# Kernel tuning notes

Hardware: AMD Instinct MI355X
Metric: run time of the kernel (lower is better)

Reference implementation:

```python
import jax, jax.numpy as jnp
import numpy as np

N = 8192
H_CHANNELS = 2048
HEADS = 16
D = H_CHANNELS // HEADS  # 128


def setup_inputs() -> dict:
    key = jax.random.key(0)
    k1, k2, k3 = jax.random.split(key, 3)
    x0 = jax.random.normal(k1, (N, H_CHANNELS), dtype=jnp.float32)
    # boolean mask: True entries are masked out (set to -inf)
    mask = jax.random.randint(k2, (N, N), 0, 2).astype(jnp.bool_)
    # torch Linear weight layout: [out_features, in_features] = [3*d, h_channels]
    W_qkv = jax.random.normal(k3, (3 * D, H_CHANNELS), dtype=jnp.float32) * (1.0 / np.sqrt(H_CHANNELS))
    return {"x0": x0, "mask": mask, "W_qkv": W_qkv}


def reference(x0, mask, W_qkv):
    # qkv = x0 @ W^T : [N, 3d]
    qkv = x0 @ W_qkv.T
    q, k, v = jnp.split(qkv, 3, axis=-1)          # each [N, d]
    att_logits = (q @ k.T) / D                    # [N, N]  (note: scale is /d, not /sqrt(d))
    att_logits = jnp.where(mask, -jnp.inf, att_logits)
    att = jax.nn.softmax(att_logits, axis=-1)     # [N, N]
    # dropout p=0.0 (eval mode) -> identity
    return att @ v                                # [N, d]
```

## Files before the change

### kernel.cpp

```cpp
#include <hip/hip_runtime.h>
#include <hip/hip_bf16.h>

typedef __attribute__((ext_vector_type(8))) short short8;
typedef __attribute__((ext_vector_type(4))) float f32x4;
typedef __attribute__((ext_vector_type(16))) float f32x16;
typedef __attribute__((ext_vector_type(2))) unsigned int uint2v;

#define NTOK 8192
#define HCH  2048
#define DDIM 128
#define NSPLIT 8
#define KPS   (NTOK / NSPLIT)
#define NITER (KPS / 64)

__device__ __forceinline__ unsigned short f2bf(float f) {
    __hip_bfloat16 h = __float2bfloat16(f);
    return *reinterpret_cast<unsigned short*>(&h);
}
__device__ __forceinline__ unsigned short f2h(float f) {
    _Float16 h = (_Float16)f;
    return *reinterpret_cast<unsigned short*>(&h);
}

__device__ __forceinline__ void gload_lds16(const void* g, void* l) {
    __builtin_amdgcn_global_load_lds(
        reinterpret_cast<const __attribute__((address_space(1))) unsigned int*>(
            reinterpret_cast<uintptr_t>(g)),
        reinterpret_cast<__attribute__((address_space(3))) unsigned int*>(
            reinterpret_cast<uintptr_t>(l)),
        16, 0, 0);
}

__global__ void detect_kernel(const unsigned int* __restrict__ X,
                              const unsigned int* __restrict__ M,
                              int* __restrict__ flags)
{
    const int lane = threadIdx.x & 63;
    unsigned int e = (X[lane] >> 7) & 0xFF;
    unsigned long long hb = __ballot(e >= 110 && e <= 140);

    bool w_ok = true, h_ok = true, b_ok = true;
#pragma unroll
    for (int i = 0; i < 16; i++) {
        unsigned int u = M[lane + 64 * i];
        if (!(u == 0u || u == 1u || u == 0x3F800000u)) w_ok = false;
        unsigned int h0 = u & 0xFFFFu, h1 = u >> 16;
        bool o0 = (h0 == 0u || h0 == 0x3F80u || h0 == 0x3C00u || h0 == 1u);
        bool o1 = (h1 == 0u || h1 == 0x3F80u || h1 == 0x3C00u || h1 == 1u);
        if (!(o0 && o1)) h_ok = false;
        unsigned int b0 = u & 0xFF, b1 = (u >> 8) & 0xFF,
                     b2 = (u >> 16) & 0xFF, b3 = u >> 24;
        if (b0 > 1u || b1 > 1u || b2 > 1u || b3 > 1u) b_ok = false;
    }
    bool allw = __all(w_ok), allh = __all(h_ok), allb = __all(b_ok);
    if (lane == 0) {
        flags[0] = (__popcll(hb) < 32) ? 1 : 0;
        flags[1] = allw ? 0 : (allb ? 1 : (allh ? 2 : 3));
    }
}

__global__ __launch_bounds__(256) void conv_w(
    const void* __restrict__ Wv, const int* __restrict__ flags,
    unsigned short* __restrict__ Wbf)
{
    int t = blockIdx.x * 256 + threadIdx.x;
    size_t off = (size_t)t * 8;
    if (flags[0] != 0) {
        const float* Wf = (const float*)Wv;
        float4 a = *reinterpret_cast<const float4*>(Wf + off);
        float4 b = *reinterpret_cast<const float4*>(Wf + off + 4);
        unsigned short o[8] = { f2bf(a.x), f2bf(a.y), f2bf(a.z), f2bf(a.w),
                                f2bf(b.x), f2bf(b.y), f2bf(b.z), f2bf(b.w) };
        *reinterpret_cast<uint4*>(Wbf + off) = *reinterpret_cast<uint4*>(o);
    } else {
        *reinterpret_cast<uint4*>(Wbf + off) =
            *reinterpret_cast<const uint4*>((const unsigned short*)Wv + off);
    }
}

__global__ __launch_bounds__(256) void conv_x(
    const void* __restrict__ Xv, const int* __restrict__ flags,
    unsigned short* __restrict__ Xbf)
{
    int t = blockIdx.x * 256 + threadIdx.x;
    size_t off = (size_t)t * 8;
    if (flags[0] != 0) {
        const float* Xf = (const float*)Xv;
        float4 a = *reinterpret_cast<const float4*>(Xf + off);
        float4 b = *reinterpret_cast<const float4*>(Xf + off + 4);
        unsigned short o[8] = { f2bf(a.x), f2bf(a.y), f2bf(a.z), f2bf(a.w),
                                f2bf(b.x), f2bf(b.y), f2bf(b.z), f2bf(b.w) };
        *reinterpret_cast<uint4*>(Xbf + off) = *reinterpret_cast<uint4*>(o);
    } else {
        *reinterpret_cast<uint4*>(Xbf + off) =
            *reinterpret_cast<const uint4*>((const unsigned short*)Xv + off);
    }
}

__global__ __launch_bounds__(256) void mask_pack(
    const void* __restrict__ maskv, const int* __restrict__ flags,
    unsigned char* __restrict__ Mp)
{
    const int mmode = flags[1];
    const int NB = NTOK * (NTOK / 8);
    int t0 = blockIdx.x * 256 + threadIdx.x;
    for (int b = t0; b < NB; b += 2048 * 256) {
        unsigned int byte = 0;
        if (mmode == 0) {
            const uint4* p = reinterpret_cast<const uint4*>(
                (const unsigned int*)maskv + (size_t)b * 8);
            uint4 a = p[0], c = p[1];
            byte = (a.x != 0u) | ((a.y != 0u) << 1) | ((a.z != 0u) << 2) | ((a.w != 0u) << 3)
                 | ((c.x != 0u) << 4) | ((c.y != 0u) << 5) | ((c.z != 0u) << 6) | ((c.w != 0u) << 7);
        } else if (mmode == 1) {
            unsigned long long v = *reinterpret_cast<const unsigned long long*>(
                (const unsigned char*)maskv + (size_t)b * 8);
#pragma unroll
            for (int k = 0; k < 8; k++)
                byte |= (((v >> (8 * k)) & 0xFFull) != 0ull) << k;
        } else if (mmode == 2) {
            uint4 a = *reinterpret_cast<const uint4*>(
                (const unsigned short*)maskv + (size_t)b * 8);
            byte = ((a.x & 0xFFFFu) != 0u) | ((a.x >> 16 != 0u) << 1)
                 | (((a.y & 0xFFFFu) != 0u) << 2) | ((a.y >> 16 != 0u) << 3)
                 | (((a.z & 0xFFFFu) != 0u) << 4) | ((a.z >> 16 != 0u) << 5)
                 | (((a.w & 0xFFFFu) != 0u) << 6) | ((a.w >> 16 != 0u) << 7);
        } else {
            byte = ((const unsigned char*)maskv)[b];
        }
        Mp[b] = (unsigned char)byte;
    }
}

__global__ __launch_bounds__(256) void qkv_gemm(
    const unsigned short* __restrict__ Xbf, const unsigned short* __restrict__ Wbf,
    unsigned short* __restrict__ Qb, unsigned short* __restrict__ Kb,
    unsigned short* __restrict__ Vb)
{
    __shared__ unsigned short Wsm[128 * 64];
    __shared__ unsigned short Xsm[32 * 64];
    const int tid  = threadIdx.x;
    const int lane = tid & 63, w = tid >> 6;
    const int c = lane & 15, g = lane >> 4;
    const int q0 = blockIdx.x * 32;
    const int n0 = blockIdx.y * 128;

    f32x4 acc[4];
#pragma unroll
    for (int i = 0; i < 4; i++) acc[i] = (f32x4){0.f, 0.f, 0.f, 0.f};

    const int xrow = tid >> 3, xc8 = tid & 7;
    const int arow = (w & 1) * 16 + c;

    for (int kk = 0; kk < HCH; kk += 64) {
        __syncthreads();
#pragma unroll
        for (int i = 0; i < 4; i++) {
            int cid = tid + 256 * i;
            int n = cid >> 3, c8 = cid & 7;
            gload_lds16(Wbf + (size_t)(n0 + n) * HCH + kk + ((c8 ^ (n & 7)) * 8),
                        &Wsm[cid * 8]);
        }
        gload_lds16(Xbf + (size_t)(q0 + xrow) * HCH + kk + ((xc8 ^ (xrow & 7)) * 8),
                    &Xsm[tid * 8]);
        __syncthreads();
#pragma unroll
        for (int ks = 0; ks < 2; ks++) {
            short8 af = *reinterpret_cast<const short8*>(
                &Xsm[(arow * 8 + ((ks * 4 + g) ^ (c & 7))) * 8]);
#pragma unroll
            for (int nt = 0; nt < 4; nt++) {
                int n = (w >> 1) * 64 + nt * 16 + c;
                short8 bf = *reinterpret_cast<const short8*>(
                    &Wsm[(n * 8 + ((ks * 4 + g) ^ (c & 7))) * 8]);
                acc[nt] = __builtin_amdgcn_mfma_f32_16x16x32_bf16(af, bf, acc[nt], 0, 0, 0);
            }
        }
    }
    unsigned short* dst = (blockIdx.y == 0) ? Qb : (blockIdx.y == 1) ? Kb : Vb;
#pragma unroll
    for (int nt = 0; nt < 4; nt++) {
        int n = (w >> 1) * 64 + nt * 16 + c;
#pragma unroll
        for (int r = 0; r < 4; r++) {
            int rr = q0 + (w & 1) * 16 + g * 4 + r;
            dst[(size_t)rr * DDIM + n] = f2bf(acc[nt][r]);
        }
    }
}

__global__ __launch_bounds__(256) void vtrans(
    const unsigned short* __restrict__ V, unsigned short* __restrict__ VT)
{
    __shared__ unsigned short T[32 * 33];
    const int t = threadIdx.x;
    const int k0 = blockIdx.x * 32, d0 = blockIdx.y * 32;
    {
        int key = t >> 3, dq = (t & 7) * 4;
        ushort4 v = *reinterpret_cast<const ushort4*>(V + (size_t)(k0 + key) * DDIM + d0 + dq);
        T[(dq + 0) * 33 + key] = v.x;
        T[(dq + 1) * 33 + key] = v.y;
        T[(dq + 2) * 33 + key] = v.z;
        T[(dq + 3) * 33 + key] = v.w;
    }
    __syncthreads();
    {
        int d = t >> 3, kq = (t & 7) * 4;
        ushort4 o;
        o.x = T[d * 33 + kq + 0]; o.y = T[d * 33 + kq + 1];
        o.z = T[d * 33 + kq + 2]; o.w = T[d * 33 + kq + 3];
        *reinterpret_cast<ushort4*>(VT + (size_t)(d0 + d) * NTOK + k0 + kq) = o;
    }
}

__global__ __launch_bounds__(256) void attn_part(
    const unsigned short* __restrict__ Qb, const unsigned short* __restrict__ Kb,
    const unsigned short* __restrict__ VT, const unsigned long long* __restrict__ Mp,
    _Float16* __restrict__ Opart, float* __restrict__ lpart)
{
    __shared__ unsigned short Ksm[2][64 * 128];
    __shared__ unsigned short Vsm[2][128 * 64];
    const int tid  = threadIdx.x;
    const int lane = tid & 63, w = tid >> 6;
    const int la = lane & 31, hi = lane >> 5;
    const int split = blockIdx.x;
    const int qb    = blockIdx.y;
    const int q0 = qb * 128;
    const int kbase = split * KPS;
    const int tb0 = kbase >> 6;
    const int qrow = q0 + w * 32 + la;

    auto stage = [&](int b, int tt) {
        const int k0s = kbase + tt * 64;
#pragma unroll
        for (int i = 0; i < 4; i++) {
            int cid = tid + 256 * i;
            int rowk = cid >> 4, c16 = cid & 15;
            gload_lds16(Kb + (size_t)(k0s + rowk) * DDIM + ((c16 ^ (rowk & 15)) * 8),
                        &Ksm[b][cid * 8]);
        }
#pragma unroll
        for (int i = 0; i < 4; i++) {
            int cid = tid + 256 * i;
            int d = cid >> 3, c8 = cid & 7;
            gload_lds16(VT + (size_t)d * NTOK + k0s + ((c8 ^ (d & 7)) * 8),
                        &Vsm[b][cid * 8]);
        }
    };

    short8 qf[8];
#pragma unroll
    for (int dstep = 0; dstep < 8; dstep++)
        qf[dstep] = *reinterpret_cast<const short8*>(
            Qb + (size_t)qrow * DDIM + dstep * 16 + hi * 8);

    f32x16 accO[4];
#pragma unroll
    for (int dt = 0; dt < 4; dt++)
#pragma unroll
        for (int r = 0; r < 16; r++) accO[dt][r] = 0.f;
    float Lacc = 0.f;

    unsigned long long mw = Mp[(size_t)qrow * 128 + tb0], mwn = 0;

    stage(0, 0);

    for (int t = 0; t < NITER; t++) {
        __syncthreads();
        if (t + 1 < NITER) {
            stage((t + 1) & 1, t + 1);
            mwn = Mp[(size_t)qrow * 128 + tb0 + t + 1];
        }
        const unsigned short* Ks = Ksm[t & 1];
        const unsigned short* Vs = Vsm[t & 1];

        f32x16 S0, S1;
#pragma unroll
        for (int r = 0; r < 16; r++) { S0[r] = 0.f; S1[r] = 0.f; }
#pragma unroll
        for (int dstep = 0; dstep < 8; dstep++) {
            int slot = (2 * dstep + hi) ^ (la & 15);
            short8 k0f = *reinterpret_cast<const short8*>(&Ks[(la * 16 + slot) * 8]);
            short8 k1f = *reinterpret_cast<const short8*>(&Ks[((32 + la) * 16 + slot) * 8]);
            S0 = __builtin_amdgcn_mfma_f32_32x32x16_bf16(k0f, qf[dstep], S0, 0, 0, 0);
            S1 = __builtin_amdgcn_mfma_f32_32x32x16_bf16(k1f, qf[dstep], S1, 0, 0, 0);
        }

        const unsigned long long mh = mw >> (4 * hi);
        short8 pa[4];
        auto softpack = [&](const f32x16& S, int kt, short8* paP) {
            float p[16];
#pragma unroll
            for (int r = 0; r < 16; r++) {
                int bit = kt * 32 + (r & 3) + 8 * (r >> 2);
                bool mv = (mh >> bit) & 1ull;
                float e = __expf(S[r] * 0.0078125f);
                p[r] = mv ? 0.f : e;
                Lacc += p[r];
            }
            unsigned int U[4][2];
#pragma unroll
            for (int b = 0; b < 4; b++) {
                asm("v_cvt_pk_bf16_f32 %0, %1, %2"
                    : "=v"(U[b][0]) : "v"(p[4 * b + 0]), "v"(p[4 * b + 1]));
                asm("v_cvt_pk_bf16_f32 %0, %1, %2"
                    : "=v"(U[b][1]) : "v"(p[4 * b + 2]), "v"(p[4 * b + 3]));
            }
#pragma unroll
            for (int h = 0; h < 2; h++) {
                uint2v sA = __builtin_amdgcn_permlane32_swap(U[2 * h][0], U[2 * h + 1][0], false, false);
                uint2v sB = __builtin_amdgcn_permlane32_swap(U[2 * h][1], U[2 * h + 1][1], false, false);
                unsigned int fr[4] = { sA.x, sB.x, sA.y, sB.y };
                paP[h] = *reinterpret_cast<short8*>(fr);
            }
        };
        softpack(S0, 0, &pa[0]);
        softpack(S1, 1, &pa[2]);

#pragma unroll
        for (int s = 0; s < 4; s++) {
#pragma unroll
            for (int dt = 0; dt < 4; dt++) {
                int slot = (2 * s + hi) ^ (la & 7);
                short8 vf = *reinterpret_cast<const short8*>(
                    &Vs[((dt * 32 + la) * 8 + slot) * 8]);
                accO[dt] = __builtin_amdgcn_mfma_f32_32x32x16_bf16(pa[s], vf, accO[dt], 0, 0, 0);
            }
        }
        if (t + 1 < NITER) mw = mwn;
    }

    Lacc += __shfl_xor(Lacc, 32, 64);

    _Float16* Ob = Opart + ((size_t)split * 64 + qb) * (128 * DDIM) + (size_t)w * 4096;
#pragma unroll
    for (int dt = 0; dt < 4; dt++)
#pragma unroll
        for (int b = 0; b < 4; b++) {
            unsigned int w0 = (unsigned int)f2h(accO[dt][4 * b + 0])
                            | ((unsigned int)f2h(accO[dt][4 * b + 1]) << 16);
            unsigned int w1 = (unsigned int)f2h(accO[dt][4 * b + 2])
                            | ((unsigned int)f2h(accO[dt][4 * b + 3]) << 16);
            uint2 uv; uv.x = w0; uv.y = w1;
            *reinterpret_cast<uint2*>(Ob + (size_t)((dt * 4 + b) * 64 + lane) * 4) = uv;
        }
    if (hi == 0)
        lpart[(size_t)split * NTOK + q0 + w * 32 + la] = Lacc;
}

__global__ __launch_bounds__(256) void combine(
    const _Float16* __restrict__ Opart, const float* __restrict__ lpart,
    float* __restrict__ out)
{
    int cid = blockIdx.x * 256 + threadIdx.x;
    int l  = cid & 63;
    int b  = (cid >> 6) & 3;
    int dt = (cid >> 8) & 3;
    int w  = (cid >> 10) & 3;
    int qb = cid >> 12;
    int la = l & 31, hi = l >> 5;
    int d  = dt * 32 + la;
    int rbase = qb * 128 + w * 32 + 8 * b + 4 * hi;
    size_t off = (size_t)qb * (128 * DDIM) + (size_t)w * 4096
               + (size_t)((dt * 4 + b) * 64 + l) * 4;
    const size_t S = (size_t)NTOK * DDIM;
    float num[4] = {0.f, 0.f, 0.f, 0.f};
    float den[4] = {0.f, 0.f, 0.f, 0.f};
#pragma unroll
    for (int s = 0; s < NSPLIT; s++) {
        uint2 v = *reinterpret_cast<const uint2*>(Opart + (size_t)s * S + off);
        const _Float16* h = reinterpret_cast<const _Float16*>(&v);
#pragma unroll
        for (int j = 0; j < 4; j++) num[j] += (float)h[j];
#pragma unroll
        for (int j = 0; j < 4; j++) den[j] += lpart[(size_t)s * NTOK + rbase + j];
    }
#pragma unroll
    for (int j = 0; j < 4; j++)
        out[(size_t)(rbase + j) * DDIM + d] = (den[j] > 0.f) ? num[j] / den[j] : 0.f;
}

extern "C" void kernel_launch(void* const* d_in, const int* in_sizes, int n_in,
                              void* d_out, int out_size, void* d_ws, size_t ws_size,
                              hipStream_t stream)
{
    const void* X = d_in[0]; const void* mask = d_in[1]; const void* W = d_in[2];
    {
        const void* x_ = nullptr; const void* m_ = nullptr; const void* w_ = nullptr;
        for (int i = 0; i < n_in; i++) {
            if (in_sizes[i] == 16777216) x_ = d_in[i];
            else if (in_sizes[i] == 67108864) m_ = d_in[i];
            else if (in_sizes[i] == 786432) w_ = d_in[i];
        }
        if (x_ && m_ && w_) { X = x_; mask = m_; W = w_; }
    }
    float* out = (float*)d_out;

    char* ws = (char*)d_ws;
    unsigned short* Qb  = (unsigned short*)(ws);
    unsigned short* Kb  = (unsigned short*)(ws + (2ull << 20));
    unsigned short* VT  = (unsigned short*)(ws + (4ull << 20));
    unsigned long long* Mpk = (unsigned long long*)(ws + (6ull << 20));
    _Float16*       Opart = (_Float16*)(ws + (14ull << 20));
    unsigned short* Wbf = (unsigned short*)(ws + (14ull << 20));
    unsigned short* Vb  = (unsigned short*)(ws + (14ull << 20) + (1536ull << 10));
    float*          lpart = (float*)(ws + (30ull << 20));
    int*            flags = (int*)(ws + (30ull << 20) + (512ull << 10));
    unsigned short* Xbf = (unsigned short*)(ws + (32ull << 20));

    detect_kernel<<<1, 64, 0, stream>>>((const unsigned int*)X, (const unsigned int*)mask, flags);
    conv_w<<<dim3(384), 256, 0, stream>>>(W, flags, Wbf);
    conv_x<<<dim3(8192), 256, 0, stream>>>(X, flags, Xbf);
    mask_pack<<<dim3(2048), 256, 0, stream>>>(mask, flags, (unsigned char*)Mpk);
    qkv_gemm<<<dim3(256, 3), 256, 0, stream>>>(Xbf, Wbf, Qb, Kb, Vb);
    vtrans<<<dim3(256, 4), 256, 0, stream>>>(Vb, VT);
    attn_part<<<dim3(NSPLIT, 64), 256, 0, stream>>>(Qb, Kb, VT, Mpk, Opart, lpart);
    combine<<<dim3(1024), 256, 0, stream>>>(Opart, lpart, out);
}
```

Before: 525.1 us.

## Double query rows per attention block to reuse staged K/V tiles

Each wave now handles two 32-row query groups, so a block covers 256 query rows instead of 128 and the grid's query dimension halves. Every K and V tile staged in shared memory therefore feeds twice as many MFMAs, halving global and LDS traffic per unit of work. The combine kernel's indexing is updated to the new partial-output layout. In exchange, register pressure roughly doubles (launch bounds set to one block per multiprocessor) and the grid shrinks to 256 blocks, which lowers occupancy and latency hiding.

After: 509.3 us. 1.03x faster.

```diff
diff --git a/kernel.cpp b/kernel.cpp
--- a/kernel.cpp
+++ b/kernel.cpp
@@ -213,7 +213,7 @@
     }
 }
 
-__global__ __launch_bounds__(256) void attn_part(
+__global__ __launch_bounds__(256, 1) void attn_part(
     const unsigned short* __restrict__ Qb, const unsigned short* __restrict__ Kb,
     const unsigned short* __restrict__ VT, const unsigned long long* __restrict__ Mp,
     _Float16* __restrict__ Opart, float* __restrict__ lpart)
@@ -225,10 +225,11 @@
     const int la = lane & 31, hi = lane >> 5;
     const int split = blockIdx.x;
     const int qb    = blockIdx.y;
-    const int q0 = qb * 128;
+    const int q0 = qb * 256;
     const int kbase = split * KPS;
     const int tb0 = kbase >> 6;
-    const int qrow = q0 + w * 32 + la;
+    const int qrowA = q0 + w * 64 + la;
+    const int qrowB = qrowA + 32;
 
     auto stage = [&](int b, int tt) {
         const int k0s = kbase + tt * 64;
@@ -248,20 +249,27 @@
         }
     };
 
-    short8 qf[8];
-#pragma unroll
-    for (int dstep = 0; dstep < 8; dstep++)
-        qf[dstep] = *reinterpret_cast<const short8*>(
-            Qb + (size_t)qrow * DDIM + dstep * 16 + hi * 8);
-
-    f32x16 accO[4];
-#pragma unroll
-    for (int dt = 0; dt < 4; dt++)
-#pragma unroll
-        for (int r = 0; r < 16; r++) accO[dt][r] = 0.f;
-    float Lacc = 0.f;
-
-    unsigned long long mw = Mp[(size_t)qrow * 128 + tb0], mwn = 0;
+    short8 qfA[8], qfB[8];
+#pragma unroll
+    for (int dstep = 0; dstep < 8; dstep++) {
+        qfA[dstep] = *reinterpret_cast<const short8*>(
+            Qb + (size_t)qrowA * DDIM + dstep * 16 + hi * 8);
+        qfB[dstep] = *reinterpret_cast<const short8*>(
+            Qb + (size_t)qrowB * DDIM + dstep * 16 + hi * 8);
+    }
+
+    f32x16 accO[2][4];
+#pragma unroll
+    for (int qh = 0; qh < 2; qh++)
+#pragma unroll
+        for (int dt = 0; dt < 4; dt++)
+#pragma unroll
+            for (int r = 0; r < 16; r++) accO[qh][dt][r] = 0.f;
+    float LaccA = 0.f, LaccB = 0.f;
+
+    unsigned long long mwA = Mp[(size_t)qrowA * 128 + tb0];
+    unsigned long long mwB = Mp[(size_t)qrowB * 128 + tb0];
+    unsigned long long mwnA = 0, mwnB = 0;
 
     stage(0, 0);
 
@@ -269,26 +277,29 @@
         __syncthreads();
         if (t + 1 < NITER) {
             stage((t + 1) & 1, t + 1);
-            mwn = Mp[(size_t)qrow * 128 + tb0 + t + 1];
+            mwnA = Mp[(size_t)qrowA * 128 + tb0 + t + 1];
+            mwnB = Mp[(size_t)qrowB * 128 + tb0 + t + 1];
         }
         const unsigned short* Ks = Ksm[t & 1];
         const unsigned short* Vs = Vsm[t & 1];
 
-        f32x16 S0, S1;
-#pragma unroll
-        for (int r = 0; r < 16; r++) { S0[r] = 0.f; S1[r] = 0.f; }
+        f32x16 S0A, S1A, S0B, S1B;
+#pragma unroll
+        for (int r = 0; r < 16; r++) { S0A[r] = 0.f; S1A[r] = 0.f; S0B[r] = 0.f; S1B[r] = 0.f; }
 #pragma unroll
         for (int dstep = 0; dstep < 8; dstep++) {
             int slot = (2 * dstep + hi) ^ (la & 15);
             short8 k0f = *reinterpret_cast<const short8*>(&Ks[(la * 16 + slot) * 8]);
             short8 k1f = *reinterpret_cast<const short8*>(&Ks[((32 + la) * 16 + slot) * 8]);
-            S0 = __builtin_amdgcn_mfma_f32_32x32x16_bf16(k0f, qf[dstep], S0, 0, 0, 0);
-            S1 = __builtin_amdgcn_mfma_f32_32x32x16_bf16(k1f, qf[dstep], S1, 0, 0, 0);
-        }
-
-        const unsigned long long mh = mw >> (4 * hi);
-        short8 pa[4];
-        auto softpack = [&](const f32x16& S, int kt, short8* paP) {
+            S0A = __builtin_amdgcn_mfma_f32_32x32x16_bf16(k0f, qfA[dstep], S0A, 0, 0, 0);
+            S1A = __builtin_amdgcn_mfma_f32_32x32x16_bf16(k1f, qfA[dstep], S1A, 0, 0, 0);
+            S0B = __builtin_amdgcn_mfma_f32_32x32x16_bf16(k0f, qfB[dstep], S0B, 0, 0, 0);
+            S1B = __builtin_amdgcn_mfma_f32_32x32x16_bf16(k1f, qfB[dstep], S1B, 0, 0, 0);
+        }
+
+        short8 paA[4], paB[4];
+        auto softpack = [&](const f32x16& S, int kt, short8* paP,
+                            unsigned long long mh, float& Lacc) {
             float p[16];
 #pragma unroll
             for (int r = 0; r < 16; r++) {
@@ -314,8 +325,12 @@
                 paP[h] = *reinterpret_cast<short8*>(fr);
             }
         };
-        softpack(S0, 0, &pa[0]);
-        softpack(S1, 1, &pa[2]);
+        const unsigned long long mhA = mwA >> (4 * hi);
+        const unsigned long long mhB = mwB >> (4 * hi);
+        softpack(S0A, 0, &paA[0], mhA, LaccA);
+        softpack(S1A, 1, &paA[2], mhA, LaccA);
+        softpack(S0B, 0, &paB[0], mhB, LaccB);
+        softpack(S1B, 1, &paB[2], mhB, LaccB);
 
 #pragma unroll
         for (int s = 0; s < 4; s++) {
@@ -324,28 +339,35 @@
                 int slot = (2 * s + hi) ^ (la & 7);
                 short8 vf = *reinterpret_cast<const short8*>(
                     &Vs[((dt * 32 + la) * 8 + slot) * 8]);
-                accO[dt] = __builtin_amdgcn_mfma_f32_32x32x16_bf16(pa[s], vf, accO[dt], 0, 0, 0);
-            }
-        }
-        if (t + 1 < NITER) mw = mwn;
-    }
-
-    Lacc += __shfl_xor(Lacc, 32, 64);
-
-    _Float16* Ob = Opart + ((size_t)split * 64 + qb) * (128 * DDIM) + (size_t)w * 4096;
-#pragma unroll
-    for (int dt = 0; dt < 4; dt++)
-#pragma unroll
-        for (int b = 0; b < 4; b++) {
-            unsigned int w0 = (unsigned int)f2h(accO[dt][4 * b + 0])
-                            | ((unsigned int)f2h(accO[dt][4 * b + 1]) << 16);
-            unsigned int w1 = (unsigned int)f2h(accO[dt][4 * b + 2])
-                            | ((unsigned int)f2h(accO[dt][4 * b + 3]) << 16);
-            uint2 uv; uv.x = w0; uv.y = w1;
-            *reinterpret_cast<uint2*>(Ob + (size_t)((dt * 4 + b) * 64 + lane) * 4) = uv;
-        }
-    if (hi == 0)
-        lpart[(size_t)split * NTOK + q0 + w * 32 + la] = Lacc;
+                accO[0][dt] = __builtin_amdgcn_mfma_f32_32x32x16_bf16(paA[s], vf, accO[0][dt], 0, 0, 0);
+                accO[1][dt] = __builtin_amdgcn_mfma_f32_32x32x16_bf16(paB[s], vf, accO[1][dt], 0, 0, 0);
+            }
+        }
+        if (t + 1 < NITER) { mwA = mwnA; mwB = mwnB; }
+    }
+
+    LaccA += __shfl_xor(LaccA, 32, 64);
+    LaccB += __shfl_xor(LaccB, 32, 64);
+
+    _Float16* Ob = Opart + ((size_t)split * 32 + qb) * (256 * DDIM) + (size_t)w * 8192;
+#pragma unroll
+    for (int qh = 0; qh < 2; qh++)
+#pragma unroll
+        for (int dt = 0; dt < 4; dt++)
+#pragma unroll
+            for (int b = 0; b < 4; b++) {
+                unsigned int w0 = (unsigned int)f2h(accO[qh][dt][4 * b + 0])
+                                | ((unsigned int)f2h(accO[qh][dt][4 * b + 1]) << 16);
+                unsigned int w1 = (unsigned int)f2h(accO[qh][dt][4 * b + 2])
+                                | ((unsigned int)f2h(accO[qh][dt][4 * b + 3]) << 16);
+                uint2 uv; uv.x = w0; uv.y = w1;
+                *reinterpret_cast<uint2*>(
+                    Ob + (size_t)((((qh * 4 + dt) * 4 + b) * 64 + lane) * 4)) = uv;
+            }
+    if (hi == 0) {
+        lpart[(size_t)split * NTOK + q0 + w * 64 + la] = LaccA;
+        lpart[(size_t)split * NTOK + q0 + w * 64 + 32 + la] = LaccB;
+    }
 }
 
 __global__ __launch_bounds__(256) void combine(
@@ -356,13 +378,14 @@
     int l  = cid & 63;
     int b  = (cid >> 6) & 3;
     int dt = (cid >> 8) & 3;
-    int w  = (cid >> 10) & 3;
-    int qb = cid >> 12;
+    int qh = (cid >> 10) & 1;
+    int w  = (cid >> 11) & 3;
+    int qb = cid >> 13;
     int la = l & 31, hi = l >> 5;
     int d  = dt * 32 + la;
-    int rbase = qb * 128 + w * 32 + 8 * b + 4 * hi;
-    size_t off = (size_t)qb * (128 * DDIM) + (size_t)w * 4096
-               + (size_t)((dt * 4 + b) * 64 + l) * 4;
+    int rbase = qb * 256 + w * 64 + qh * 32 + 8 * b + 4 * hi;
+    size_t off = (size_t)qb * (256 * DDIM) + (size_t)w * 8192
+               + (size_t)((((qh * 4 + dt) * 4 + b) * 64 + l) * 4);
     const size_t S = (size_t)NTOK * DDIM;
     float num[4] = {0.f, 0.f, 0.f, 0.f};
     float den[4] = {0.f, 0.f, 0.f, 0.f};
@@ -414,6 +437,6 @@
     mask_pack<<<dim3(2048), 256, 0, stream>>>(mask, flags, (unsigned char*)Mpk);
     qkv_gemm<<<dim3(256, 3), 256, 0, stream>>>(Xbf, Wbf, Qb, Kb, Vb);
     vtrans<<<dim3(256, 4), 256, 0, stream>>>(Vb, VT);
-    attn_part<<<dim3(NSPLIT, 64), 256, 0, stream>>>(Qb, Kb, VT, Mpk, Opart, lpart);
+    attn_part<<<dim3(NSPLIT, 32), 256, 0, stream>>>(Qb, Kb, VT, Mpk, Opart, lpart);
     combine<<<dim3(1024), 256, 0, stream>>>(Opart, lpart, out);
 }
```
